# Kernel tuning notes

Measured on AMD Instinct MI355X. Metric: run time of the kernel, lower is better.

The kernel has to match this reference:

```python
import jax, jax.numpy as jnp
import numpy as np

L, B, S, D, H, DK, F = 6, 4, 2048, 512, 8, 64, 2048


def setup_inputs() -> dict:
    key = jax.random.key(0)
    ks = iter(jax.random.split(key, 40))
    def rn(shape, scale=0.02):
        return jax.random.normal(next(ks), shape, jnp.float32) * scale
    inp = {
        "x": jax.random.normal(next(ks), (B, S, D), jnp.float32),
        "enc": jax.random.normal(next(ks), (B, S, D), jnp.float32),
    }
    for pre in ("sa", "ca"):
        inp[f"{pre}_wq"] = rn((L, D, H * DK)); inp[f"{pre}_bq"] = jnp.zeros((L, H * DK), jnp.float32)
        inp[f"{pre}_wk"] = rn((L, D, H * DK)); inp[f"{pre}_bk"] = jnp.zeros((L, H * DK), jnp.float32)
        inp[f"{pre}_wv"] = rn((L, D, H * DK)); inp[f"{pre}_bv"] = jnp.zeros((L, H * DK), jnp.float32)
        inp[f"{pre}_wo"] = rn((L, H * DK, D)); inp[f"{pre}_bo"] = jnp.zeros((L, D), jnp.float32)
    for i in (1, 2, 3):
        inp[f"ln{i}_g"] = jnp.ones((L, D), jnp.float32)
        inp[f"ln{i}_b"] = jnp.zeros((L, D), jnp.float32)
    inp["ff_w1"] = rn((L, D, F)); inp["ff_b1"] = jnp.zeros((L, F), jnp.float32)
    inp["ff_w2"] = rn((L, F, D)); inp["ff_b2"] = jnp.zeros((L, D), jnp.float32)
    return inp


def _layer_norm(z, g, b, eps=1e-5):
    m = z.mean(-1, keepdims=True)
    v = z.var(-1, keepdims=True)
    return (z - m) * jax.lax.rsqrt(v + eps) * g + b


def _mha(q_in, kv_in, wq, bq, wk, bk, wv, bv, wo, bo, causal_bias):
    b, s, _ = q_in.shape
    Q = (q_in @ wq + bq).reshape(b, s, H, DK)   # [B,S,H,DK]
    K = (kv_in @ wk + bk).reshape(b, s, H, DK)
    V = (kv_in @ wv + bv).reshape(b, s, H, DK)
    scores = jnp.einsum("bqhd,bkhd->bhqk", Q, K) / jnp.float32(DK) ** 0.5
    if causal_bias is not None:
        scores = scores + causal_bias  # additive -inf above diagonal
    w = jax.nn.softmax(scores, axis=-1)
    att = jnp.einsum("bhqk,bkhd->bqhd", w, V).reshape(b, s, H * DK)
    return att @ wo + bo


def reference(x, enc, sa_wq, sa_bq, sa_wk, sa_bk, sa_wv, sa_bv, sa_wo, sa_bo,
              ca_wq, ca_bq, ca_wk, ca_bk, ca_wv, ca_bv, ca_wo, ca_bo,
              ln1_g, ln1_b, ln2_g, ln2_b, ln3_g, ln3_b,
              ff_w1, ff_b1, ff_w2, ff_b2):
    s = x.shape[1]
    causal_bias = jnp.triu(jnp.full((s, s), -jnp.inf, jnp.float32), 1)

    params = (sa_wq, sa_bq, sa_wk, sa_bk, sa_wv, sa_bv, sa_wo, sa_bo,
              ca_wq, ca_bq, ca_wk, ca_bk, ca_wv, ca_bv, ca_wo, ca_bo,
              ln1_g, ln1_b, ln2_g, ln2_b, ln3_g, ln3_b,
              ff_w1, ff_b1, ff_w2, ff_b2)

    def block(h, p):
        (swq, sbq, swk, sbk, swv, sbv, swo, sbo,
         cwq, cbq, cwk, cbk, cwv, cbv, cwo, cbo,
         g1, b1, g2, b2, g3, b3, w1, bb1, w2, bb2) = p
        # masked self-attention + residual + LN  (faithful to source)
        x1 = _layer_norm(h + _mha(h, h, swq, sbq, swk, sbk, swv, sbv, swo, sbo, causal_bias), g1, b1)
        # cross-attention; residual comes from the BLOCK INPUT h (source bug kept)
        y = _layer_norm(h + _mha(x1, enc, cwq, cbq, cwk, cbk, cwv, cbv, cwo, cbo, None), g2, b2)
        # FFN; residual from x1 (source bug kept)
        out = _layer_norm(x1 + (jax.nn.relu(y @ w1 + bb1) @ w2 + bb2), g3, b3)
        return out, None

    out, _ = jax.lax.scan(block, x, params)
    return out
```

## Files before the change

kernel.cpp:

```cpp
#include <hip/hip_runtime.h>
#include <stdint.h>

#define LCOUNT 6
#define BB 4
#define SS 2048
#define DD 512
#define HH 8
#define DKK 64
#define FFDIM 2048
#define MM (BB*SS)

typedef __attribute__((ext_vector_type(8))) __bf16 bf16x8;
typedef __attribute__((ext_vector_type(4))) float f32x4;
typedef unsigned short u16;

__device__ __forceinline__ u16 f2bf(float f) {
  union { __bf16 h; u16 u; } v; v.h = (__bf16)f; return v.u;
}
__device__ __forceinline__ float bf2f(u16 u) {
  union { uint32_t u; float f; } v; v.u = ((uint32_t)u) << 16;
  return v.f;
}

__device__ __forceinline__ void gload_lds16(const u16* gsrc, u16* ldst) {
  __builtin_amdgcn_global_load_lds((const __attribute__((address_space(1))) char*)gsrc,
                                   (__attribute__((address_space(3))) char*)ldst, 16, 0, 0);
}

__global__ __launch_bounds__(256) void f2bf_kernel(const float* __restrict__ in,
                                                   u16* __restrict__ outp, int n) {
  int i = (blockIdx.x * 256 + threadIdx.x) * 8;
  if (i >= n) return;
  float4 a = *(const float4*)&in[i];
  float4 b = *(const float4*)&in[i + 4];
  union { u16 us[8]; uint4 v; } pk;
  pk.us[0] = f2bf(a.x); pk.us[1] = f2bf(a.y); pk.us[2] = f2bf(a.z); pk.us[3] = f2bf(a.w);
  pk.us[4] = f2bf(b.x); pk.us[5] = f2bf(b.y); pk.us[6] = f2bf(b.z); pk.us[7] = f2bf(b.w);
  *(uint4*)&outp[i] = pk.v;
}

__global__ __launch_bounds__(256) void bias_cat(const float* a, const float* b, const float* c,
                                                float* dst, int n, int total) {
  int i = blockIdx.x * 256 + threadIdx.x;
  if (i >= total) return;
  int parts = (c != nullptr) ? 3 : 2;
  int per = parts * n;
  int l = i / per, cc = i % per;
  const float* s = cc < n ? a : (cc < 2 * n ? b : c);
  dst[i] = s[l * n + (cc % n)];
}

__global__ __launch_bounds__(256) void wtrans(const float* __restrict__ W,
                                              u16* __restrict__ Wt, int K_, int N_,
                                              size_t lstride) {
  __shared__ float tile[64 * 65];
  const int l = blockIdx.z;
  const float* Wl = W + (size_t)l * K_ * N_;
  u16* Wtl = Wt + (size_t)l * lstride;
  const int n0 = blockIdx.x * 64, k0 = blockIdx.y * 64;
  const int tid = threadIdx.x;
  const int r = tid >> 2, c4 = (tid & 3) * 16;
#pragma unroll
  for (int j = 0; j < 16; j += 4) {
    float4 v = *(const float4*)&Wl[(size_t)(k0 + r) * N_ + n0 + c4 + j];
    tile[r * 65 + c4 + j + 0] = v.x;
    tile[r * 65 + c4 + j + 1] = v.y;
    tile[r * 65 + c4 + j + 2] = v.z;
    tile[r * 65 + c4 + j + 3] = v.w;
  }
  __syncthreads();
  const int nr = tid >> 2, kc = (tid & 3) * 16;
#pragma unroll
  for (int half = 0; half < 2; ++half) {
    union { u16 us[8]; uint4 v; } pk;
#pragma unroll
    for (int e = 0; e < 8; ++e) pk.us[e] = f2bf(tile[(kc + half * 8 + e) * 65 + nr]);
    *(uint4*)&Wtl[(size_t)(n0 + nr) * K_ + k0 + kc + half * 8] = pk.v;
  }
}

template <int BMT, bool RELU, bool VT>
__global__ __launch_bounds__(256)
void gemm_bt(const u16* __restrict__ A, const u16* __restrict__ Bt,
             const float* __restrict__ bias, u16* __restrict__ C,
             int N_, int K_, int CS, u16* __restrict__ vt, int vtc0) {
  constexpr int MR = BMT / 32;
  __shared__ u16 As[BMT * 64];
  __shared__ u16 Bs[128 * 64];
  const int tid = threadIdx.x;
  const int wid = tid >> 6, lane = tid & 63;
  const int l15 = lane & 15, g = lane >> 4;
  const int wr = wid >> 1, wc = wid & 1;
  const int lin = blockIdx.x + gridDim.x * blockIdx.y;
  const int nwg = gridDim.x * gridDim.y;
  const int swz = (lin & 7) * (nwg >> 3) + (lin >> 3);
  const int brow = (swz / gridDim.x) * BMT;
  const int bcol = (swz % gridDim.x) * 128;

  f32x4 acc[MR][4];
#pragma unroll
  for (int m = 0; m < MR; ++m)
#pragma unroll
    for (int n = 0; n < 4; ++n) acc[m][n] = (f32x4){0.f, 0.f, 0.f, 0.f};

  for (int kt = 0; kt < K_; kt += 64) {
#pragma unroll
    for (int r = 0; r < BMT / 32; ++r) {
      int row = r * 32 + wid * 8 + (lane >> 3);
      int slot = (lane & 7) ^ (row & 7);
      gload_lds16(A + (size_t)(brow + row) * K_ + kt + slot * 8,
                  &As[r * 2048 + wid * 512]);
    }
#pragma unroll
    for (int r = 0; r < 4; ++r) {
      int row = r * 32 + wid * 8 + (lane >> 3);
      int slot = (lane & 7) ^ (row & 7);
      gload_lds16(Bt + (size_t)(bcol + row) * K_ + kt + slot * 8,
                  &Bs[r * 2048 + wid * 512]);
    }
    __syncthreads();
#pragma unroll
    for (int ks = 0; ks < 2; ++ks) {
      bf16x8 af[MR], bfr[4];
#pragma unroll
      for (int m = 0; m < MR; ++m) {
        int row = wr * (BMT / 2) + m * 16 + l15;
        int slot = (ks * 4 + g) ^ (row & 7);
        af[m] = *(const bf16x8*)&As[row * 64 + slot * 8];
      }
#pragma unroll
      for (int n = 0; n < 4; ++n) {
        int row = wc * 64 + n * 16 + l15;
        int slot = (ks * 4 + g) ^ (row & 7);
        bfr[n] = *(const bf16x8*)&Bs[row * 64 + slot * 8];
      }
#pragma unroll
      for (int m = 0; m < MR; ++m)
#pragma unroll
        for (int n = 0; n < 4; ++n)
          acc[m][n] = __builtin_amdgcn_mfma_f32_16x16x32_bf16(af[m], bfr[n], acc[m][n], 0, 0, 0);
    }
    __syncthreads();
  }
#pragma unroll
  for (int n = 0; n < 4; ++n) {
    int col = bcol + wc * 64 + n * 16 + l15;
    float bv = bias ? bias[col] : 0.f;
    if (VT && col >= vtc0) {
      int hh = (col - vtc0) >> 6, dd = (col - vtc0) & 63;
#pragma unroll
      for (int m = 0; m < MR; ++m) {
        int s0g = brow + wr * (BMT / 2) + m * 16 + g * 4;
        int bb = s0g >> 11, ss = s0g & (SS - 1);
        union { u16 us[4]; uint2 v; } pk;
#pragma unroll
        for (int r = 0; r < 4; ++r) pk.us[r] = f2bf(acc[m][n][r] + bv);
        *(uint2*)&vt[(((size_t)(bb * HH + hh)) * DKK + dd) * SS + ss] = pk.v;
      }
    } else {
#pragma unroll
      for (int m = 0; m < MR; ++m) {
#pragma unroll
        for (int r = 0; r < 4; ++r) {
          int rowg = brow + wr * (BMT / 2) + m * 16 + g * 4 + r;
          float v = acc[m][n][r] + bv;
          if (RELU) v = fmaxf(v, 0.f);
          C[(size_t)rowg * CS + col] = f2bf(v);
        }
      }
    }
  }
}

template <bool CAUSAL>
__global__ __launch_bounds__(256, 4)
void attn_kernel(const u16* __restrict__ Qm, const u16* __restrict__ Km,
                 const u16* __restrict__ Vt, u16* __restrict__ Om, int qks) {
  __shared__ u16 Ks[2][64 * 64];
  __shared__ u16 Vs[2][64 * 64];
  __shared__ u16 Ps[4][16 * 64];
  const int lin = blockIdx.x;
  const int bh = (lin & 7) * 4 + ((lin >> 3) >> 5);
  const int qb = (lin >> 3) & 31;
  const int h = bh & 7, b = bh >> 3;
  const int tid = threadIdx.x, wid = tid >> 6, lane = tid & 63;
  const int l15 = lane & 15, g = lane >> 4;
  const int qstart = qb * 64;
  const size_t qbase = ((size_t)b * SS) * qks + h * DKK;
  const size_t vtbase = (size_t)(b * HH + h) * DKK * SS;
  const size_t obase = ((size_t)b * SS) * DD + h * DKK;
  u16* psw = &Ps[wid][0];
  const int srow = wid * 8 + (lane >> 3);
  const int sslot = lane & 7;
  const int qg = qstart + wid * 16 + l15;
  const int pswz = (l15 & 7) << 1;
  const float SC = 0.18033688f;

  bf16x8 qf[2];
#pragma unroll
  for (int ks = 0; ks < 2; ++ks)
    qf[ks] = *(const bf16x8*)&Qm[qbase + (size_t)qg * qks + ks * 32 + g * 8];

  f32x4 oacc[4];
#pragma unroll
  for (int nb = 0; nb < 4; ++nb) oacc[nb] = (f32x4){0.f, 0.f, 0.f, 0.f};
  float m_run = -3.0e38f, l_run = 0.f;

  const int T = CAUSAL ? (qb + 1) : (SS / 64);

#pragma unroll
  for (int r = 0; r < 2; ++r) {
    int row = r * 32 + srow;
    int slot = sslot ^ (row & 7);
    gload_lds16(Km + qbase + (size_t)row * qks + slot * 8, &Ks[0][r * 2048 + wid * 512]);
    gload_lds16(Vt + vtbase + (size_t)row * SS + slot * 8, &Vs[0][r * 2048 + wid * 512]);
  }
  __syncthreads();

  int cur = 0;
  for (int t = 0; t < T; ++t) {
    const int kstart = t * 64;
    if (t + 1 < T) {
#pragma unroll
      for (int r = 0; r < 2; ++r) {
        int row = r * 32 + srow;
        int slot = sslot ^ (row & 7);
        gload_lds16(Km + qbase + (size_t)(kstart + 64 + row) * qks + slot * 8,
                    &Ks[cur ^ 1][r * 2048 + wid * 512]);
        gload_lds16(Vt + vtbase + (size_t)row * SS + kstart + 64 + slot * 8,
                    &Vs[cur ^ 1][r * 2048 + wid * 512]);
      }
    }
    f32x4 sacc[4];
#pragma unroll
    for (int nb = 0; nb < 4; ++nb) sacc[nb] = (f32x4){0.f, 0.f, 0.f, 0.f};
#pragma unroll
    for (int nb = 0; nb < 4; ++nb) {
      int row = nb * 16 + l15;
#pragma unroll
      for (int ks = 0; ks < 2; ++ks) {
        bf16x8 kf = *(const bf16x8*)&Ks[cur][row * 64 + (((ks * 4 + g) ^ (row & 7)) * 8)];
        sacc[nb] = __builtin_amdgcn_mfma_f32_16x16x32_bf16(kf, qf[ks], sacc[nb], 0, 0, 0);
      }
    }
    if (CAUSAL && t == T - 1) {
#pragma unroll
      for (int nb = 0; nb < 4; ++nb)
#pragma unroll
        for (int r = 0; r < 4; ++r)
          if ((kstart + nb * 16 + g * 4 + r) > qg) sacc[nb][r] = -3.0e38f;
    }
    f32x4 m4 = sacc[0];
#pragma unroll
    for (int nb = 1; nb < 4; ++nb) {
      m4[0] = fmaxf(m4[0], sacc[nb][0]); m4[1] = fmaxf(m4[1], sacc[nb][1]);
      m4[2] = fmaxf(m4[2], sacc[nb][2]); m4[3] = fmaxf(m4[3], sacc[nb][3]);
    }
    float mx = fmaxf(fmaxf(m4[0], m4[1]), fmaxf(m4[2], m4[3]));
    mx = fmaxf(mx, __shfl_xor(mx, 16));
    mx = fmaxf(mx, __shfl_xor(mx, 32));
    const bool skip = __all(mx <= m_run + 64.0f);
    float mnew = skip ? m_run : fmaxf(m_run, mx);
    float mc = mnew * SC;
    float s = 0.f;
#pragma unroll
    for (int nb = 0; nb < 4; ++nb) {
#pragma unroll
      for (int r = 0; r < 4; ++r) {
        float e = __builtin_amdgcn_exp2f(sacc[nb][r] * SC - mc);
        sacc[nb][r] = e; s += e;
      }
    }
    s += __shfl_xor(s, 16);
    s += __shfl_xor(s, 32);
    if (skip) {
      l_run += s;
    } else {
      float resc = __builtin_amdgcn_exp2f((m_run - mnew) * SC);
      l_run = l_run * resc + s;
      m_run = mnew;
      float ro[4];
#pragma unroll
      for (int r = 0; r < 4; ++r) ro[r] = __shfl(resc, g * 4 + r);
#pragma unroll
      for (int nb = 0; nb < 4; ++nb)
#pragma unroll
        for (int r = 0; r < 4; ++r) oacc[nb][r] *= ro[r];
    }
#pragma unroll
    for (int nb = 0; nb < 4; ++nb) {
      union { u16 us[4]; uint2 v; } pk;
#pragma unroll
      for (int r = 0; r < 4; ++r) pk.us[r] = f2bf(sacc[nb][r]);
      int cp = (nb * 4 + g) ^ pswz;
      *(uint2*)&psw[l15 * 64 + cp * 4] = pk.v;
    }
    bf16x8 pf[2];
#pragma unroll
    for (int ks = 0; ks < 2; ++ks) {
      int cp0 = (8 * ks + 2 * g) ^ pswz;
      pf[ks] = *(const bf16x8*)&psw[l15 * 64 + cp0 * 4];
    }
#pragma unroll
    for (int nb = 0; nb < 4; ++nb) {
      int row = nb * 16 + l15;
#pragma unroll
      for (int ks = 0; ks < 2; ++ks) {
        bf16x8 vf = *(const bf16x8*)&Vs[cur][row * 64 + (((ks * 4 + g) ^ (row & 7)) * 8)];
        oacc[nb] = __builtin_amdgcn_mfma_f32_16x16x32_bf16(pf[ks], vf, oacc[nb], 0, 0, 0);
      }
    }
    __syncthreads();
    cur ^= 1;
  }
  float linv = 1.f / l_run;
  float io[4];
#pragma unroll
  for (int r = 0; r < 4; ++r) io[r] = __shfl(linv, g * 4 + r);
#pragma unroll
  for (int nb = 0; nb < 4; ++nb) {
#pragma unroll
    for (int r = 0; r < 4; ++r) {
      Om[obase + (size_t)(qstart + wid * 16 + g * 4 + r) * DD + nb * 16 + l15] =
          f2bf(oacc[nb][r] * io[r]);
    }
  }
}

__global__ __launch_bounds__(256)
void ln_kernel(const u16* __restrict__ A, const u16* __restrict__ Bv,
               const float* __restrict__ gamma, const float* __restrict__ beta,
               u16* __restrict__ out_bf, float* __restrict__ out_f32) {
  const int row = blockIdx.x * 4 + (threadIdx.x >> 6);
  const int lane = threadIdx.x & 63;
  uint4 av = *(const uint4*)&A[(size_t)row * DD + lane * 8];
  uint4 bv = *(const uint4*)&Bv[(size_t)row * DD + lane * 8];
  const u16* au = (const u16*)&av;
  const u16* bu = (const u16*)&bv;
  float z[8], s = 0.f, s2 = 0.f;
#pragma unroll
  for (int j = 0; j < 8; ++j) {
    float x = bf2f(au[j]) + bf2f(bu[j]);
    z[j] = x; s += x; s2 += x * x;
  }
#pragma unroll
  for (int off = 1; off < 64; off <<= 1) {
    s += __shfl_xor(s, off);
    s2 += __shfl_xor(s2, off);
  }
  float mean = s * (1.f / 512.f);
  float var = s2 * (1.f / 512.f) - mean * mean;
  float rs = rsqrtf(var + 1e-5f);
  union { u16 us[8]; uint4 v; } pk;
#pragma unroll
  for (int j = 0; j < 8; ++j) {
    float o = (z[j] - mean) * rs * gamma[lane * 8 + j] + beta[lane * 8 + j];
    pk.us[j] = f2bf(o);
    if (out_f32) out_f32[(size_t)row * DD + lane * 8 + j] = o;
  }
  *(uint4*)&out_bf[(size_t)row * DD + lane * 8] = pk.v;
}

extern "C" void kernel_launch(void* const* d_in, const int* in_sizes, int n_in,
                              void* d_out, int out_size, void* d_ws, size_t ws_size,
                              hipStream_t stream) {
  const float* x   = (const float*)d_in[0];
  const float* enc = (const float*)d_in[1];
  const float* sa_w[4] = {(const float*)d_in[2], (const float*)d_in[4], (const float*)d_in[6], (const float*)d_in[8]};
  const float* sa_b[4] = {(const float*)d_in[3], (const float*)d_in[5], (const float*)d_in[7], (const float*)d_in[9]};
  const float* ca_w[4] = {(const float*)d_in[10], (const float*)d_in[12], (const float*)d_in[14], (const float*)d_in[16]};
  const float* ca_b[4] = {(const float*)d_in[11], (const float*)d_in[13], (const float*)d_in[15], (const float*)d_in[17]};
  const float* ln_g[3] = {(const float*)d_in[18], (const float*)d_in[20], (const float*)d_in[22]};
  const float* ln_b[3] = {(const float*)d_in[19], (const float*)d_in[21], (const float*)d_in[23]};
  const float* ffw1 = (const float*)d_in[24];
  const float* ffb1 = (const float*)d_in[25];
  const float* ffw2 = (const float*)d_in[26];
  const float* ffb2 = (const float*)d_in[27];

  char* ws = (char*)d_ws;
  size_t o = 0;
  auto take = [&](size_t bytes) {
    void* p = ws + o;
    o += (bytes + 255) & ~(size_t)255;
    return p;
  };
  u16* wqkv  = (u16*)take((size_t)LCOUNT * 1536 * 512 * 2);
  u16* wqca  = (u16*)take((size_t)LCOUNT * 512 * 512 * 2);
  u16* wkvca = (u16*)take((size_t)LCOUNT * 1024 * 512 * 2);
  u16* wosa  = (u16*)take((size_t)LCOUNT * 512 * 512 * 2);
  u16* woca  = (u16*)take((size_t)LCOUNT * 512 * 512 * 2);
  u16* w1t   = (u16*)take((size_t)LCOUNT * 512 * 2048 * 2);
  u16* w2t   = (u16*)take((size_t)LCOUNT * 2048 * 512 * 2);
  float* bqkv = (float*)take((size_t)LCOUNT * 1536 * 4);
  float* bkv  = (float*)take((size_t)LCOUNT * 1024 * 4);
  u16* Hb   = (u16*)take((size_t)MM * 512 * 2);
  u16* Eb   = (u16*)take((size_t)MM * 512 * 2);
  u16* QKVb = (u16*)take((size_t)MM * 1536 * 2);
  u16* Ab   = (u16*)take((size_t)MM * 512 * 2);
  u16* Pb   = (u16*)take((size_t)MM * 512 * 2);
  u16* X1b  = (u16*)take((size_t)MM * 512 * 2);
  u16* Yb   = (u16*)take((size_t)MM * 512 * 2);
  u16* Fb   = (u16*)take((size_t)MM * 2048 * 2);
  u16* Vtb  = Fb;

  f2bf_kernel<<<2048, 256, 0, stream>>>(x, Hb, MM * 512);
  f2bf_kernel<<<2048, 256, 0, stream>>>(enc, Eb, MM * 512);
  wtrans<<<dim3(8, 8, LCOUNT), 256, 0, stream>>>(sa_w[0], wqkv,              512, 512, (size_t)1536 * 512);
  wtrans<<<dim3(8, 8, LCOUNT), 256, 0, stream>>>(sa_w[1], wqkv + 512 * 512,  512, 512, (size_t)1536 * 512);
  wtrans<<<dim3(8, 8, LCOUNT), 256, 0, stream>>>(sa_w[2], wqkv + 1024 * 512, 512, 512, (size_t)1536 * 512);
  wtrans<<<dim3(8, 8, LCOUNT), 256, 0, stream>>>(sa_w[3], wosa,              512, 512, (size_t)512 * 512);
  wtrans<<<dim3(8, 8, LCOUNT), 256, 0, stream>>>(ca_w[0], wqca,              512, 512, (size_t)512 * 512);
  wtrans<<<dim3(8, 8, LCOUNT), 256, 0, stream>>>(ca_w[1], wkvca,             512, 512, (size_t)1024 * 512);
  wtrans<<<dim3(8, 8, LCOUNT), 256, 0, stream>>>(ca_w[2], wkvca + 512 * 512, 512, 512, (size_t)1024 * 512);
  wtrans<<<dim3(8, 8, LCOUNT), 256, 0, stream>>>(ca_w[3], woca,              512, 512, (size_t)512 * 512);
  wtrans<<<dim3(32, 8, LCOUNT), 256, 0, stream>>>(ffw1, w1t, 512, 2048, (size_t)2048 * 512);
  wtrans<<<dim3(8, 32, LCOUNT), 256, 0, stream>>>(ffw2, w2t, 2048, 512, (size_t)512 * 2048);
  bias_cat<<<36, 256, 0, stream>>>(sa_b[0], sa_b[1], sa_b[2], bqkv, 512, LCOUNT * 1536);
  bias_cat<<<24, 256, 0, stream>>>(ca_b[1], ca_b[2], nullptr, bkv, 512, LCOUNT * 1024);

  for (int l = 0; l < LCOUNT; ++l) {
    const size_t w512 = (size_t)l * 512 * 512;
    const size_t wff = (size_t)l * 512 * 2048;
    gemm_bt<128, false, true><<<dim3(12, 64), 256, 0, stream>>>(
        Hb, wqkv + (size_t)l * 1536 * 512, bqkv + l * 1536, QKVb, 1536, 512, 1536, Vtb, 1024);
    attn_kernel<true><<<dim3(1024), 256, 0, stream>>>(QKVb, QKVb + 512, Vtb, Ab, 1536);
    gemm_bt<64, false, false><<<dim3(4, 128), 256, 0, stream>>>(
        Ab, wosa + w512, sa_b[3] + l * 512, Pb, 512, 512, 512, nullptr, 0);
    ln_kernel<<<MM / 4, 256, 0, stream>>>(Hb, Pb, ln_g[0] + l * 512, ln_b[0] + l * 512, X1b, nullptr);
    gemm_bt<64, false, false><<<dim3(4, 128), 256, 0, stream>>>(
        X1b, wqca + w512, ca_b[0] + l * 512, QKVb, 512, 512, 1536, nullptr, 0);
    gemm_bt<128, false, true><<<dim3(8, 64), 256, 0, stream>>>(
        Eb, wkvca + (size_t)l * 1024 * 512, bkv + l * 1024, QKVb + 512, 1024, 512, 1536, Vtb, 512);
    attn_kernel<false><<<dim3(1024), 256, 0, stream>>>(QKVb, QKVb + 512, Vtb, Ab, 1536);
    gemm_bt<64, false, false><<<dim3(4, 128), 256, 0, stream>>>(
        Ab, woca + w512, ca_b[3] + l * 512, Pb, 512, 512, 512, nullptr, 0);
    ln_kernel<<<MM / 4, 256, 0, stream>>>(Hb, Pb, ln_g[1] + l * 512, ln_b[1] + l * 512, Yb, nullptr);
    gemm_bt<128, true, false><<<dim3(16, 64), 256, 0, stream>>>(
        Yb, w1t + wff, ffb1 + l * 2048, Fb, 2048, 512, 2048, nullptr, 0);
    gemm_bt<64, false, false><<<dim3(4, 128), 256, 0, stream>>>(
        Fb, w2t + wff, ffb2 + l * 512, Pb, 512, 2048, 512, nullptr, 0);
    ln_kernel<<<MM / 4, 256, 0, stream>>>(X1b, Pb, ln_g[2] + l * 512, ln_b[2] + l * 512, Hb,
                                          (l == LCOUNT - 1) ? (float*)d_out : nullptr);
  }
}
```

Measured before the change: 1.900 ms.

## Stage attention K/V tiles through registers into single LDS buffer, reorder causal blocks

Replaces the double-buffered direct global-to-LDS K/V loads with register prefetch into a single LDS buffer, written after a barrier at the end of each tile. This halves the attention kernel's LDS footprint so the occupancy hint is raised from 4 to 6 blocks per CU. It also interleaves query-block indices (long and short causal rows alternate) to balance work across the grid. The cost is an extra barrier per tile, more VGPR pressure from the staged registers, and less overlap because the LDS store waits for the compute to finish.

New measurement: 2.794 ms. 47.0% more time.

```diff
diff --git a/kernel.cpp b/kernel.cpp
--- a/kernel.cpp
+++ b/kernel.cpp
@@ -173,15 +173,16 @@
 }
 
 template <bool CAUSAL>
-__global__ __launch_bounds__(256, 4)
+__global__ __launch_bounds__(256, 6)
 void attn_kernel(const u16* __restrict__ Qm, const u16* __restrict__ Km,
                  const u16* __restrict__ Vt, u16* __restrict__ Om, int qks) {
-  __shared__ u16 Ks[2][64 * 64];
-  __shared__ u16 Vs[2][64 * 64];
+  __shared__ u16 Ks[64 * 64];
+  __shared__ u16 Vs[64 * 64];
   __shared__ u16 Ps[4][16 * 64];
   const int lin = blockIdx.x;
   const int bh = (lin & 7) * 4 + ((lin >> 3) >> 5);
-  const int qb = (lin >> 3) & 31;
+  const int qc = (lin >> 3) & 31;
+  const int qb = (qc & 1) ? (31 - (qc >> 1)) : (qc >> 1);
   const int h = bh & 7, b = bh >> 3;
   const int tid = threadIdx.x, wid = tid >> 6, lane = tid & 63;
   const int l15 = lane & 15, g = lane >> 4;
@@ -196,6 +197,9 @@
   const int pswz = (l15 & 7) << 1;
   const float SC = 0.18033688f;
 
+  const u16* kp = Km + qbase;
+  const u16* vp = Vt + vtbase;
+
   bf16x8 qf[2];
 #pragma unroll
   for (int ks = 0; ks < 2; ++ks)
@@ -208,27 +212,30 @@
 
   const int T = CAUSAL ? (qb + 1) : (SS / 64);
 
+  uint4 kreg[2], vreg[2];
 #pragma unroll
   for (int r = 0; r < 2; ++r) {
     int row = r * 32 + srow;
-    int slot = sslot ^ (row & 7);
-    gload_lds16(Km + qbase + (size_t)row * qks + slot * 8, &Ks[0][r * 2048 + wid * 512]);
-    gload_lds16(Vt + vtbase + (size_t)row * SS + slot * 8, &Vs[0][r * 2048 + wid * 512]);
+    kreg[r] = *(const uint4*)&kp[(size_t)row * qks + sslot * 8];
+    vreg[r] = *(const uint4*)&vp[(size_t)row * SS + sslot * 8];
+  }
+#pragma unroll
+  for (int r = 0; r < 2; ++r) {
+    int row = r * 32 + srow;
+    int d = row * 64 + ((sslot ^ (row & 7)) * 8);
+    *(uint4*)&Ks[d] = kreg[r];
+    *(uint4*)&Vs[d] = vreg[r];
   }
   __syncthreads();
 
-  int cur = 0;
   for (int t = 0; t < T; ++t) {
     const int kstart = t * 64;
     if (t + 1 < T) {
 #pragma unroll
       for (int r = 0; r < 2; ++r) {
         int row = r * 32 + srow;
-        int slot = sslot ^ (row & 7);
-        gload_lds16(Km + qbase + (size_t)(kstart + 64 + row) * qks + slot * 8,
-                    &Ks[cur ^ 1][r * 2048 + wid * 512]);
-        gload_lds16(Vt + vtbase + (size_t)row * SS + kstart + 64 + slot * 8,
-                    &Vs[cur ^ 1][r * 2048 + wid * 512]);
+        kreg[r] = *(const uint4*)&kp[(size_t)(kstart + 64 + row) * qks + sslot * 8];
+        vreg[r] = *(const uint4*)&vp[(size_t)row * SS + kstart + 64 + sslot * 8];
       }
     }
     f32x4 sacc[4];
@@ -239,7 +246,7 @@
       int row = nb * 16 + l15;
 #pragma unroll
       for (int ks = 0; ks < 2; ++ks) {
-        bf16x8 kf = *(const bf16x8*)&Ks[cur][row * 64 + (((ks * 4 + g) ^ (row & 7)) * 8)];
+        bf16x8 kf = *(const bf16x8*)&Ks[row * 64 + (((ks * 4 + g) ^ (row & 7)) * 8)];
         sacc[nb] = __builtin_amdgcn_mfma_f32_16x16x32_bf16(kf, qf[ks], sacc[nb], 0, 0, 0);
       }
     }
@@ -306,12 +313,21 @@
       int row = nb * 16 + l15;
 #pragma unroll
       for (int ks = 0; ks < 2; ++ks) {
-        bf16x8 vf = *(const bf16x8*)&Vs[cur][row * 64 + (((ks * 4 + g) ^ (row & 7)) * 8)];
+        bf16x8 vf = *(const bf16x8*)&Vs[row * 64 + (((ks * 4 + g) ^ (row & 7)) * 8)];
         oacc[nb] = __builtin_amdgcn_mfma_f32_16x16x32_bf16(pf[ks], vf, oacc[nb], 0, 0, 0);
       }
     }
-    __syncthreads();
-    cur ^= 1;
+    if (t + 1 < T) {
+      __syncthreads();
+#pragma unroll
+      for (int r = 0; r < 2; ++r) {
+        int row = r * 32 + srow;
+        int d = row * 64 + ((sslot ^ (row & 7)) * 8);
+        *(uint4*)&Ks[d] = kreg[r];
+        *(uint4*)&Vs[d] = vreg[r];
+      }
+      __syncthreads();
+    }
   }
   float linv = 1.f / l_run;
   float io[4];
```
